# Performance work log

Hardware: AMD Instinct MI355X
Metric: run time of the kernel (lower is better)

## Reference

```python
import jax, jax.numpy as jnp
import numpy as np

K = 3          # kernel_size (forced by hardcoded padding=1 in query unfold)
PAD = 1        # padding
C_IN = 64      # conv in_channels (x has C_IN + 5 channels)
C_OUT = 128    # out_channels
B, H, W = 16, 32, 32


def unfold(x, k, pad=0, mode='constant'):
    """torch.nn.functional.unfold equivalent. x: (B,C,H,W) -> (B, C*k*k, L).
    Ordering matches torch: channel slowest, then kernel row, then kernel col."""
    if pad:
        x = jnp.pad(x, ((0, 0), (0, 0), (pad, pad), (pad, pad)), mode=mode)
    b, c, h, w = x.shape
    oh, ow = h - k + 1, w - k + 1
    # (B, C, k*k, oh, ow) with patch index i*k+j
    patches = jnp.stack([x[:, :, i:i + oh, j:j + ow]
                         for i in range(k) for j in range(k)], axis=2)
    return patches.reshape(b, c * k * k, oh * ow)


def conv2d(x, w, b, pad):
    out = jax.lax.conv_general_dilated(
        x, w, window_strides=(1, 1), padding=[(pad, pad), (pad, pad)],
        dimension_numbers=('NCHW', 'OIHW', 'NCHW'))
    return out + b[None, :, None, None]


def setup_inputs() -> dict:
    key = jax.random.key(0)
    ks = jax.random.split(key, 6)
    fan1 = C_IN * K * K
    fan2 = C_OUT * 1 * 1
    return {
        'x': jax.random.normal(ks[0], (B, C_IN + 5, H, W), jnp.float32),
        'conv_w': jax.random.normal(ks[1], (C_OUT, C_IN, K, K), jnp.float32) / np.sqrt(fan1),
        'conv_b': jax.random.normal(ks[2], (C_OUT,), jnp.float32) * 0.01,
        'conv2_w': jax.random.normal(ks[3], (1, C_OUT, 1, 1), jnp.float32) / np.sqrt(fan2),
        'conv2_b': jax.random.normal(ks[4], (1,), jnp.float32) * 0.01,
        'shapes_kernel': jax.random.uniform(ks[5], (1, C_OUT, K * K * 5, 1), jnp.float32),
    }


def reference(x, conv_w, conv_b, conv2_w, conv2_b, shapes_kernel):
    k, pad = K, PAD
    center = k * k // 2

    conv_out = conv2d(x[:, :-5], conv_w, conv_b, pad)          # (B, C_OUT, H', W')
    b, cout, oh, ow = conv_out.shape
    L = oh * ow

    # shape-channel windows (replication-padded), center-relative positions
    sw = unfold(x[:, -5:], k, pad, 'edge').reshape(b, 5, k * k, L)
    sw = sw.at[:, 0:2].add(-sw[:, 0:2, center:center + 1])

    # L1 distance of each window to each learned shape kernel
    sd = jnp.abs(sw.reshape(b, 1, 5 * k * k, L) - shapes_kernel).sum(axis=2)  # (B, C_OUT, L)
    sd = sd.reshape(b, cout, oh, ow)

    saf = jax.nn.relu(conv_out / (sd + 1.0))                    # shape_attended_features

    q = conv2d(saf, conv2_w, conv2_b, 0) / jnp.sqrt(jnp.float32(cout))  # (B, 1, H', W')
    qu = jax.nn.softmax(unfold(q, k, 1), axis=1)[:, None]       # (B, 1, k*k, L), zero-padded

    u_mean = unfold(x[:, -5:-3], k, pad, 'edge').reshape(b, 2, k * k, L)
    means = (u_mean * qu).sum(axis=2)                           # (B, 2, L)

    v1 = (unfold(x[:, -3:-1], k, pad, 'edge').reshape(b, 2, k * k, L) * qu).sum(axis=2)
    v2 = (((u_mean - means[:, :, None, :]) ** 2) * qu).sum(axis=2)
    var = v1 + v2                                               # (B, 2, L)

    c1 = (unfold(x[:, -1:], k, pad, 'edge').reshape(b, 1, k * k, L) * qu).sum(axis=2)
    c2 = ((u_mean[:, 0:1] - means[:, 0:1, None, :]) *
          (u_mean[:, 1:2] - means[:, 1:2, None, :]) * qu).sum(axis=2)
    covar = c1 + c2                                             # (B, 1, L)

    agg = jnp.concatenate([means, var, covar], axis=1).reshape(b, 5, oh, ow)
    return jnp.concatenate([saf, agg], axis=1)                  # (B, C_OUT+5, H', W')
```

## Files before the change

kernel.cpp:

```cpp
#include <hip/hip_runtime.h>
#include <math.h>

#define CI 64
#define CO 128
#define CX 69
#define LPIX 1024

typedef __attribute__((ext_vector_type(8))) short bf16x8;
typedef __attribute__((ext_vector_type(4))) float f32x4;

#define XT_OFF   0
#define WMF_OFF  (2*1024*1024)
#define SKT_OFF  (WMF_OFF + 147456)
#define QP_OFF   (SKT_OFF + 23040)

__device__ __forceinline__ unsigned short f2bf(float f) {
  unsigned u = __float_as_uint(f);
  unsigned r = (u + 0x7fffu + ((u >> 16) & 1u)) >> 16;
  return (unsigned short)r;
}

__launch_bounds__(256)
__global__ void prep(const float* __restrict__ xg,
                     const float* __restrict__ cwg,
                     const float* __restrict__ skg,
                     unsigned short* __restrict__ xT,
                     unsigned short* __restrict__ wmf,
                     float* __restrict__ skt) {
  __shared__ float t[64][65];
  const int tid = threadIdx.x;
  if (blockIdx.x < 256) {
    const int b  = blockIdx.x >> 4;
    const int p0 = (blockIdx.x & 15) * 64;
    const float* xb = xg + (size_t)b * CX * LPIX;
    #pragma unroll
    for (int k = 0; k < 16; ++k) {
      int idx = tid + k * 256;
      int ci = idx >> 6, pxl = idx & 63;
      t[ci][pxl] = xb[ci * LPIX + p0 + pxl];
    }
    __syncthreads();
    const int pxl = tid >> 2, ci0 = (tid & 3) * 16;
    unsigned int pk[8];
    #pragma unroll
    for (int i = 0; i < 8; ++i) {
      unsigned short lo = f2bf(t[ci0 + 2 * i][pxl]);
      unsigned short hi = f2bf(t[ci0 + 2 * i + 1][pxl]);
      pk[i] = (unsigned)lo | ((unsigned)hi << 16);
    }
    uint4* dst = (uint4*)(xT + ((size_t)b * 1024 + p0 + pxl) * 64 + ci0);
    dst[0] = make_uint4(pk[0], pk[1], pk[2], pk[3]);
    dst[1] = make_uint4(pk[4], pk[5], pk[6], pk[7]);
  } else {
    int i = (blockIdx.x - 256) * 256 + tid;
    if (i < 9 * 128 * 64) {
      int tap = i >> 13;
      int rem = i & 8191;
      int co = rem >> 6, cis = rem & 63;
      int ci = cis ^ ((co & 7) << 3);
      wmf[i] = f2bf(cwg[co * 576 + ci * 9 + tap]);
    } else {
      int d = i - 9 * 128 * 64;
      if (d < 45 * 128) {
        int j = d >> 7, co = d & 127;
        skt[j * 128 + co] = skg[co * 45 + j];
      }
    }
  }
}

__launch_bounds__(256, 3)
__global__ void convFused(const unsigned short* __restrict__ xT,
                          const unsigned short* __restrict__ wmf,
                          const float* __restrict__ xg,
                          const float* __restrict__ cbg,
                          const float* __restrict__ w2g,
                          const float* __restrict__ sktg,
                          float* __restrict__ qp,
                          float* __restrict__ outg) {
  __shared__ char arena[16384];
  __shared__ float lds_sx[5 * 144];
  __shared__ float qred[4][64];

  unsigned short* A0 = (unsigned short*)arena;
  float* lds_c = (float*)arena;

  const int tid = threadIdx.x;
  const int blk = blockIdx.x;
  const int coh = blk & 1;
  const int rp  = (blk >> 1) & 15;
  const int b   = blk >> 5;
  const int r0  = rp * 2;

  const int w    = tid >> 6;
  const int lane = tid & 63;
  const int rsel = w >> 1;
  const int cq   = w & 1;
  const int prow = r0 + rsel;
  const int n16  = lane & 15;
  const int kq   = lane >> 4;

  const float* xs = xg + ((size_t)b * CX + CI) * LPIX;
  for (int idx = tid; idx < 5 * 144; idx += 256) {
    int c = idx / 144, rem = idx - c * 144;
    int s = rem / 36, j = rem - s * 36;
    int hh = r0 - 1 + s; hh = hh < 0 ? 0 : (hh > 31 ? 31 : hh);
    int col = j - 1;     col = col < 0 ? 0 : (col > 31 ? 31 : col);
    lds_sx[idx] = xs[c * LPIX + hh * 32 + col];
  }

  {
    const uint4* s = (const uint4*)(wmf + (size_t)(coh * 64) * 64);
    uint4 v0 = s[tid], v1 = s[tid + 256];
    uint4* d = (uint4*)A0;
    d[tid] = v0; d[tid + 256] = v1;
  }
  __syncthreads();

  f32x4 acc[2][2] = {};
  const unsigned short* xTb = xT + (size_t)b * 65536;
  const bf16x8 bzero = {};

  for (int tap = 0; tap < 9; ++tap) {
    const int dr = tap / 3, dc = tap % 3;
    uint4 pf0, pf1;
    if (tap < 8) {
      const uint4* s = (const uint4*)(wmf + (size_t)((tap + 1) * 128 + coh * 64) * 64);
      pf0 = s[tid]; pf1 = s[tid + 256];
    }
    const int row_g = prow + dr - 1;
    if ((unsigned)row_g < 32u) {
      const int c0 = n16 + dc - 1;
      const int c1 = 16 + n16 + dc - 1;
      const bool ok0 = (c0 >= 0);
      const bool ok1 = (c1 <= 31);
      const unsigned short* bp0 = xTb + (row_g * 32 + (ok0 ? c0 : 0)) * 64;
      const unsigned short* bp1 = xTb + (row_g * 32 + (ok1 ? c1 : 31)) * 64;
      const unsigned short* abase = A0 + (tap & 1) * 4096;
      #pragma unroll
      for (int ci0 = 0; ci0 < 64; ci0 += 32) {
        const int cib = ci0 + kq * 8;
        bf16x8 b0 = *(const bf16x8*)(bp0 + cib);
        bf16x8 b1 = *(const bf16x8*)(bp1 + cib);
        if (!ok0) b0 = bzero;
        if (!ok1) b1 = bzero;
        const int gs = ((kq | (ci0 >> 3)) ^ (n16 & 7)) << 3;
        #pragma unroll
        for (int ct = 0; ct < 2; ++ct) {
          const int co_l = cq * 32 + ct * 16 + n16;
          bf16x8 a = *(const bf16x8*)(abase + co_l * 64 + gs);
          acc[0][ct] = __builtin_amdgcn_mfma_f32_16x16x32_bf16(a, b0, acc[0][ct], 0, 0, 0);
          acc[1][ct] = __builtin_amdgcn_mfma_f32_16x16x32_bf16(a, b1, acc[1][ct], 0, 0, 0);
        }
      }
    }
    if (tap < 8) {
      uint4* d = (uint4*)(A0 + ((tap + 1) & 1) * 4096);
      d[tid] = pf0; d[tid + 256] = pf1;
    }
    __syncthreads();
  }

  #pragma unroll
  for (int pt = 0; pt < 2; ++pt) {
    const int pxl = rsel * 32 + pt * 16 + n16;
    #pragma unroll
    for (int ct = 0; ct < 2; ++ct) {
      const int cog = cq * 8 + ct * 4 + kq;
      const int sg  = cog ^ (pxl & 7);
      *(f32x4*)&lds_c[pxl * 64 + sg * 4] = acc[pt][ct];
    }
  }
  __syncthreads();

  const int wS   = __builtin_amdgcn_readfirstlane(w);
  const int co0g = coh * 64 + wS * 16;
  const int pxl  = lane;

  float cvals[16];
  #pragma unroll
  for (int g = 0; g < 4; ++g) {
    const int cog = wS * 4 + g;
    const int sg  = cog ^ (pxl & 7);
    *(f32x4*)&cvals[g * 4] = *(const f32x4*)&lds_c[pxl * 64 + sg * 4];
  }

  const int xbase = (pxl >> 5) * 36 + (pxl & 31);
  float swv[45];
  {
    const float c0 = lds_sx[0 * 144 + 37 + xbase];
    const float c1 = lds_sx[1 * 144 + 37 + xbase];
    #pragma unroll
    for (int c = 0; c < 5; ++c) {
      float ctr = (c == 0) ? c0 : ((c == 1) ? c1 : 0.f);
      #pragma unroll
      for (int s = 0; s < 3; ++s)
        #pragma unroll
        for (int dc = 0; dc < 3; ++dc)
          swv[c * 9 + s * 3 + dc] = lds_sx[c * 144 + s * 36 + dc + xbase] - ctr;
    }
  }

  float sd[16];
  #pragma unroll
  for (int k = 0; k < 16; ++k) sd[k] = 0.f;
  const float* skt = sktg + co0g;
  #pragma unroll
  for (int j = 0; j < 45; ++j) {
    const float sv = swv[j];
    #pragma unroll
    for (int k = 0; k < 16; ++k)
      sd[k] += fabsf(sv - skt[j * 128 + k]);
  }

  float qpv = 0.f;
  float* ob = outg + ((size_t)b * 133 + co0g) * LPIX + (r0 + (pxl >> 5)) * 32 + (pxl & 31);
  #pragma unroll
  for (int k = 0; k < 16; ++k) {
    float v = (cvals[k] + cbg[co0g + k]) * __builtin_amdgcn_rcpf(sd[k] + 1.0f);
    v = v > 0.f ? v : 0.f;
    ob[(size_t)k * LPIX] = v;
    qpv = fmaf(v, w2g[co0g + k], qpv);
  }

  qred[w][lane] = qpv;
  __syncthreads();
  if (tid < 64) {
    float q = qred[0][tid] + qred[1][tid] + qred[2][tid] + qred[3][tid];
    qp[coh * 16384 + b * LPIX + r0 * 32 + tid] = q;
  }
}

__launch_bounds__(64)
__global__ void statsB(const float* __restrict__ xg,
                       const float* __restrict__ qp,
                       const float* __restrict__ b2g,
                       float* __restrict__ outg) {
  const int gid = blockIdx.x * 64 + threadIdx.x;
  const int b = gid >> 10;
  const int h = (gid >> 5) & 31;
  const int w = gid & 31;

  const float b2 = b2g[0];
  const float* q0 = qp + (size_t)b * LPIX;
  float qv[9];
  float m = -1e30f;
  #pragma unroll
  for (int t = 0; t < 9; ++t) {
    int hh = h + t / 3 - 1, wc = w + t % 3 - 1;
    float v = 0.f;
    if ((unsigned)hh < 32u && (unsigned)wc < 32u) {
      int off = hh * 32 + wc;
      v = (q0[off] + q0[16384 + off] + b2) * 0.08838834764831845f;
    }
    qv[t] = v;
    m = fmaxf(m, v);
  }
  float ssum = 0.f;
  #pragma unroll
  for (int t = 0; t < 9; ++t) { qv[t] = expf(qv[t] - m); ssum += qv[t]; }
  const float inv = 1.f / ssum;

  const float* xs = xg + ((size_t)b * CX + CI) * LPIX;
  float um0[9], um1[9];
  float m0 = 0.f, m1 = 0.f, v1a = 0.f, v1b = 0.f, c1 = 0.f;
  #pragma unroll
  for (int t = 0; t < 9; ++t) {
    int hh = h + t / 3 - 1; hh = hh < 0 ? 0 : (hh > 31 ? 31 : hh);
    int wc = w + t % 3 - 1; wc = wc < 0 ? 0 : (wc > 31 ? 31 : wc);
    int off = hh * 32 + wc;
    float quv = qv[t] * inv;
    qv[t] = quv;
    float a0 = xs[off];
    float a1 = xs[LPIX + off];
    float b0 = xs[2 * LPIX + off];
    float b1 = xs[3 * LPIX + off];
    float cc = xs[4 * LPIX + off];
    um0[t] = a0; um1[t] = a1;
    m0 = fmaf(a0, quv, m0);
    m1 = fmaf(a1, quv, m1);
    v1a = fmaf(b0, quv, v1a);
    v1b = fmaf(b1, quv, v1b);
    c1 = fmaf(cc, quv, c1);
  }
  float var0 = v1a, var1 = v1b, cov = c1;
  #pragma unroll
  for (int t = 0; t < 9; ++t) {
    float d0 = um0[t] - m0, d1 = um1[t] - m1;
    var0 = fmaf(d0 * d0, qv[t], var0);
    var1 = fmaf(d1 * d1, qv[t], var1);
    cov  = fmaf(d0 * d1, qv[t], cov);
  }
  float* ob = outg + ((size_t)b * 133 + 128) * LPIX + h * 32 + w;
  ob[0 * LPIX] = m0;
  ob[1 * LPIX] = m1;
  ob[2 * LPIX] = var0;
  ob[3 * LPIX] = var1;
  ob[4 * LPIX] = cov;
}

extern "C" void kernel_launch(void* const* d_in, const int* in_sizes, int n_in,
                              void* d_out, int out_size, void* d_ws, size_t ws_size,
                              hipStream_t stream) {
  const float* x  = (const float*)d_in[0];
  const float* cw = (const float*)d_in[1];
  const float* cb = (const float*)d_in[2];
  const float* w2 = (const float*)d_in[3];
  const float* b2 = (const float*)d_in[4];
  const float* sk = (const float*)d_in[5];
  float* out = (float*)d_out;

  unsigned short* xT  = (unsigned short*)((char*)d_ws + XT_OFF);
  unsigned short* wmf = (unsigned short*)((char*)d_ws + WMF_OFF);
  float* skt = (float*)((char*)d_ws + SKT_OFF);
  float* qp  = (float*)((char*)d_ws + QP_OFF);

  prep<<<dim3(567), dim3(256), 0, stream>>>(x, cw, sk, xT, wmf, skt);
  convFused<<<dim3(512), dim3(256), 0, stream>>>(xT, wmf, x, cb, w2, skt, qp, out);
  statsB<<<dim3(256), dim3(64), 0, stream>>>(x, qp, b2, out);
}
```

Before: 36.60 us.

## Fuse input transpose/bf16 conversion into conv kernel via LDS halo tile

```diff
diff --git a/kernel.cpp b/kernel.cpp
--- a/kernel.cpp
+++ b/kernel.cpp
@@ -9,10 +9,9 @@
 typedef __attribute__((ext_vector_type(8))) short bf16x8;
 typedef __attribute__((ext_vector_type(4))) float f32x4;
 
-#define XT_OFF   0
-#define WMF_OFF  (2*1024*1024)
-#define SKT_OFF  (WMF_OFF + 147456)
-#define QP_OFF   (SKT_OFF + 23040)
+#define WMF_OFF  0
+#define SKT_OFF  147456
+#define QP_OFF   (147456 + 23040)
 
 __device__ __forceinline__ unsigned short f2bf(float f) {
   unsigned u = __float_as_uint(f);
@@ -21,64 +20,36 @@
 }
 
 __launch_bounds__(256)
-__global__ void prep(const float* __restrict__ xg,
-                     const float* __restrict__ cwg,
-                     const float* __restrict__ skg,
-                     unsigned short* __restrict__ xT,
-                     unsigned short* __restrict__ wmf,
-                     float* __restrict__ skt) {
-  __shared__ float t[64][65];
-  const int tid = threadIdx.x;
-  if (blockIdx.x < 256) {
-    const int b  = blockIdx.x >> 4;
-    const int p0 = (blockIdx.x & 15) * 64;
-    const float* xb = xg + (size_t)b * CX * LPIX;
-    #pragma unroll
-    for (int k = 0; k < 16; ++k) {
-      int idx = tid + k * 256;
-      int ci = idx >> 6, pxl = idx & 63;
-      t[ci][pxl] = xb[ci * LPIX + p0 + pxl];
-    }
-    __syncthreads();
-    const int pxl = tid >> 2, ci0 = (tid & 3) * 16;
-    unsigned int pk[8];
-    #pragma unroll
-    for (int i = 0; i < 8; ++i) {
-      unsigned short lo = f2bf(t[ci0 + 2 * i][pxl]);
-      unsigned short hi = f2bf(t[ci0 + 2 * i + 1][pxl]);
-      pk[i] = (unsigned)lo | ((unsigned)hi << 16);
-    }
-    uint4* dst = (uint4*)(xT + ((size_t)b * 1024 + p0 + pxl) * 64 + ci0);
-    dst[0] = make_uint4(pk[0], pk[1], pk[2], pk[3]);
-    dst[1] = make_uint4(pk[4], pk[5], pk[6], pk[7]);
+__global__ void prepW(const float* __restrict__ cwg,
+                      const float* __restrict__ skg,
+                      unsigned short* __restrict__ wmf,
+                      float* __restrict__ skt) {
+  int i = blockIdx.x * 256 + threadIdx.x;
+  if (i < 9 * 128 * 64) {
+    int tap = i >> 13;
+    int rem = i & 8191;
+    int co = rem >> 6, cis = rem & 63;
+    int ci = cis ^ ((co & 7) << 3);
+    wmf[i] = f2bf(cwg[co * 576 + ci * 9 + tap]);
   } else {
-    int i = (blockIdx.x - 256) * 256 + tid;
-    if (i < 9 * 128 * 64) {
-      int tap = i >> 13;
-      int rem = i & 8191;
-      int co = rem >> 6, cis = rem & 63;
-      int ci = cis ^ ((co & 7) << 3);
-      wmf[i] = f2bf(cwg[co * 576 + ci * 9 + tap]);
-    } else {
-      int d = i - 9 * 128 * 64;
-      if (d < 45 * 128) {
-        int j = d >> 7, co = d & 127;
-        skt[j * 128 + co] = skg[co * 45 + j];
-      }
+    int d = i - 9 * 128 * 64;
+    if (d < 45 * 128) {
+      int j = d >> 7, co = d & 127;
+      skt[j * 128 + co] = skg[co * 45 + j];
     }
   }
 }
 
 __launch_bounds__(256, 3)
-__global__ void convFused(const unsigned short* __restrict__ xT,
+__global__ void convFused(const float* __restrict__ xg,
                           const unsigned short* __restrict__ wmf,
-                          const float* __restrict__ xg,
                           const float* __restrict__ cbg,
                           const float* __restrict__ w2g,
                           const float* __restrict__ sktg,
                           float* __restrict__ qp,
                           float* __restrict__ outg) {
   __shared__ char arena[16384];
+  __shared__ unsigned short ldsB[4 * 36 * 64];
   __shared__ float lds_sx[5 * 144];
   __shared__ float qred[4][64];
 
@@ -96,11 +67,42 @@
   const int lane = tid & 63;
   const int rsel = w >> 1;
   const int cq   = w & 1;
-  const int prow = r0 + rsel;
   const int n16  = lane & 15;
   const int kq   = lane >> 4;
 
-  const float* xs = xg + ((size_t)b * CX + CI) * LPIX;
+  const float* xb = xg + (size_t)b * CX * LPIX;
+  const float* xs = xb + CI * LPIX;
+
+  {
+    const int col = tid & 31;
+    const int grp = tid >> 5;
+    const int slot = col + 1;
+    const int swk = (slot & 7) << 3;
+    #pragma unroll
+    for (int it = 0; it < 16; ++it) {
+      const int rc  = grp + it * 8;
+      const int row = rc >> 5;
+      const int ci  = (rc & 31) * 2;
+      const int grow = r0 - 1 + row;
+      unsigned v = 0;
+      if ((unsigned)grow < 32u) {
+        float f0 = xb[ci * LPIX + grow * 32 + col];
+        float f1 = xb[(ci + 1) * LPIX + grow * 32 + col];
+        v = (unsigned)f2bf(f0) | ((unsigned)f2bf(f1) << 16);
+      }
+      const int gslot = ((ci >> 3) << 3) ^ swk;
+      ((unsigned*)ldsB)[(((row * 36 + slot) << 6) + gslot + (ci & 7)) >> 1] = v;
+    }
+    for (int idx = tid; idx < 512; idx += 256) {
+      const int row = idx >> 7;
+      const int s4  = (idx >> 5) & 3;
+      const int sl  = (s4 == 0) ? 0 : (32 + s4);
+      const int ci  = (idx & 31) * 2;
+      const int gsl = ((ci >> 3) << 3) ^ ((sl & 7) << 3);
+      ((unsigned*)ldsB)[(((row * 36 + sl) << 6) + gsl + (ci & 7)) >> 1] = 0;
+    }
+  }
+
   for (int idx = tid; idx < 5 * 144; idx += 256) {
     int c = idx / 144, rem = idx - c * 144;
     int s = rem / 36, j = rem - s * 36;
@@ -118,8 +120,6 @@
   __syncthreads();
 
   f32x4 acc[2][2] = {};
-  const unsigned short* xTb = xT + (size_t)b * 65536;
-  const bf16x8 bzero = {};
 
   for (int tap = 0; tap < 9; ++tap) {
     const int dr = tap / 3, dc = tap % 3;
@@ -128,30 +128,25 @@
       const uint4* s = (const uint4*)(wmf + (size_t)((tap + 1) * 128 + coh * 64) * 64);
       pf0 = s[tid]; pf1 = s[tid + 256];
     }
-    const int row_g = prow + dr - 1;
-    if ((unsigned)row_g < 32u) {
-      const int c0 = n16 + dc - 1;
-      const int c1 = 16 + n16 + dc - 1;
-      const bool ok0 = (c0 >= 0);
-      const bool ok1 = (c1 <= 31);
-      const unsigned short* bp0 = xTb + (row_g * 32 + (ok0 ? c0 : 0)) * 64;
-      const unsigned short* bp1 = xTb + (row_g * 32 + (ok1 ? c1 : 31)) * 64;
-      const unsigned short* abase = A0 + (tap & 1) * 4096;
+    const int rowst = rsel + dr;
+    const unsigned short* abase = A0 + (tap & 1) * 4096;
+    #pragma unroll
+    for (int ci0 = 0; ci0 < 64; ci0 += 32) {
+      const int g = (ci0 >> 3) + kq;
+      bf16x8 bfr[2];
       #pragma unroll
-      for (int ci0 = 0; ci0 < 64; ci0 += 32) {
-        const int cib = ci0 + kq * 8;
-        bf16x8 b0 = *(const bf16x8*)(bp0 + cib);
-        bf16x8 b1 = *(const bf16x8*)(bp1 + cib);
-        if (!ok0) b0 = bzero;
-        if (!ok1) b1 = bzero;
-        const int gs = ((kq | (ci0 >> 3)) ^ (n16 & 7)) << 3;
-        #pragma unroll
-        for (int ct = 0; ct < 2; ++ct) {
-          const int co_l = cq * 32 + ct * 16 + n16;
-          bf16x8 a = *(const bf16x8*)(abase + co_l * 64 + gs);
-          acc[0][ct] = __builtin_amdgcn_mfma_f32_16x16x32_bf16(a, b0, acc[0][ct], 0, 0, 0);
-          acc[1][ct] = __builtin_amdgcn_mfma_f32_16x16x32_bf16(a, b1, acc[1][ct], 0, 0, 0);
-        }
+      for (int t = 0; t < 2; ++t) {
+        const int slot = t * 16 + n16 + dc;
+        const int gs = (g ^ (slot & 7)) << 3;
+        bfr[t] = *(const bf16x8*)(ldsB + ((rowst * 36 + slot) << 6) + gs);
+      }
+      const int gsa = ((kq | (ci0 >> 3)) ^ (n16 & 7)) << 3;
+      #pragma unroll
+      for (int ct = 0; ct < 2; ++ct) {
+        const int co_l = cq * 32 + ct * 16 + n16;
+        bf16x8 a = *(const bf16x8*)(abase + co_l * 64 + gsa);
+        acc[0][ct] = __builtin_amdgcn_mfma_f32_16x16x32_bf16(a, bfr[0], acc[0][ct], 0, 0, 0);
+        acc[1][ct] = __builtin_amdgcn_mfma_f32_16x16x32_bf16(a, bfr[1], acc[1][ct], 0, 0, 0);
       }
     }
     if (tap < 8) {
@@ -310,12 +305,11 @@
   const float* sk = (const float*)d_in[5];
   float* out = (float*)d_out;
 
-  unsigned short* xT  = (unsigned short*)((char*)d_ws + XT_OFF);
   unsigned short* wmf = (unsigned short*)((char*)d_ws + WMF_OFF);
   float* skt = (float*)((char*)d_ws + SKT_OFF);
   float* qp  = (float*)((char*)d_ws + QP_OFF);
 
-  prep<<<dim3(567), dim3(256), 0, stream>>>(x, cw, sk, xT, wmf, skt);
-  convFused<<<dim3(512), dim3(256), 0, stream>>>(xT, wmf, x, cb, w2, skt, qp, out);
+  prepW<<<dim3(311), dim3(256), 0, stream>>>(cw, sk, wmf, skt);
+  convFused<<<dim3(512), dim3(256), 0, stream>>>(x, wmf, cb, w2, skt, qp, out);
   statsB<<<dim3(256), dim3(64), 0, stream>>>(x, qp, b2, out);
 }
```

New measurement: 32.18 us. -12.1%, faster.
